# Optimization experiments

Hardware: AMD Instinct MI355X
Metric: run time of the kernel (lower is better)

## Reference

```python
import jax, jax.numpy as jnp
import numpy as np

MAX_DISP = 24  # 192 // (2**(3+1)/2**1)


def build_cost_volume(feat_l, feat_r, max_disp=MAX_DISP):
    # Faithful to the torch loop: cost[:, d, :, x] = sum_c |feat_l[..,x] - feat_r[..,x-d]|
    # with feat_r treated as zero for x < d (matches feat_l.abs().sum(1) branch).
    B, C, h, w = feat_l.shape
    pad = jnp.pad(feat_r, ((0, 0), (0, 0), (0, 0), (max_disp - 1, 0)))  # zero left-pad
    # idx[d, x] = x - d shifted into padded coords; x-d < 0 hits the zero pad.
    idx = (max_disp - 1) + jnp.arange(w)[None, :] - jnp.arange(max_disp)[:, None]  # [D, w]
    shifted = pad[:, :, :, idx]  # [B, C, h, D, w]
    cost = jnp.abs(feat_l[:, :, :, None, :] - shifted).sum(axis=1)  # [B, h, D, w]
    return jnp.transpose(cost, (0, 2, 1, 3))  # [B, D, h, w]


def bilinear_resize_align_corners(x, H, W):
    # F.interpolate(mode='bilinear', align_corners=True)
    B, C, h, w = x.shape
    ys = jnp.linspace(0.0, h - 1.0, H)
    xs = jnp.linspace(0.0, w - 1.0, W)
    y0 = jnp.floor(ys).astype(jnp.int32)
    y1 = jnp.minimum(y0 + 1, h - 1)
    wy = (ys - y0)[:, None]                 # [H, 1]
    x0 = jnp.floor(xs).astype(jnp.int32)
    x1 = jnp.minimum(x0 + 1, w - 1)
    wx = xs - x0                             # [W]
    rows = x[:, :, y0, :] * (1.0 - wy) + x[:, :, y1, :] * wy   # [B, C, H, w]
    out = rows[:, :, :, x0] * (1.0 - wx) + rows[:, :, :, x1] * wx  # [B, C, H, W]
    return out


def setup_inputs() -> dict:
    key = jax.random.key(0)
    k1, k2 = jax.random.split(key)
    B, C, h, w = 16, 4, 128, 240  # features at 1/8 of a 1024x1920 stereo pair
    feat_l = jax.random.normal(k1, (B, C, h, w), dtype=jnp.float32)
    feat_r = jax.random.normal(k2, (B, C, h, w), dtype=jnp.float32)
    return {"feat_l": feat_l, "feat_r": feat_r, "img_h": 1024, "img_w": 1920}


def reference(feat_l, feat_r, img_h, img_w):
    cost = build_cost_volume(feat_l, feat_r)            # [B, D, h, w]
    p = jax.nn.softmax(-cost, axis=1)                   # softmax over disparity bins
    disp = jnp.arange(MAX_DISP, dtype=feat_l.dtype).reshape(1, -1, 1, 1)
    pred = jnp.sum(p * disp, axis=1, keepdims=True)     # [B, 1, h, w]
    pred = pred * (float(img_h) / pred.shape[2])        # rescale disparity to full-res units
    return bilinear_resize_align_corners(pred, img_h, img_w)  # [B, 1, img_h, img_w]
```

## Files before the change

kernel.cpp:

```cpp
#include <hip/hip_runtime.h>
#include <math.h>

#define BB 16
#define CC 4
#define HH 128
#define WW 240
#define MAXD 24
#define OH 1024
#define OW 1920

__global__ __launch_bounds__(256) void fused_kernel(const float* __restrict__ fl,
                                                    const float* __restrict__ fr,
                                                    float* __restrict__ out) {
    const int blk = blockIdx.x;
    const int b = blk >> 7;
    const int y0 = blk & (HH - 1);
    const int y1 = min(y0 + 1, HH - 1);
    const int tid = threadIdx.x;

    __shared__ union {
        float sR[2][CC][WW + MAXD - 1];
        float vx[2][OW];
    } u;
    __shared__ float sP[2][WW];

    const int rows2[2] = {y0, y1};

    float lv[2][CC];
    #pragma unroll
    for (int t = 0; t < 2; ++t) {
        const int j = tid + t * 256;
        if (j < 2 * WW) {
            const int r = j / WW;
            const int x = j - r * WW;
            const size_t g = (((size_t)b * CC) * HH + rows2[r]) * WW + x;
            #pragma unroll
            for (int c = 0; c < CC; ++c)
                lv[t][c] = fl[g + (size_t)c * HH * WW];
        }
    }

    for (int i = tid; i < 2 * CC * WW; i += 256) {
        const int r = i / (CC * WW);
        const int rem = i - r * (CC * WW);
        const int c = rem / WW;
        const int x = rem - c * WW;
        u.sR[r][c][x + MAXD - 1] = fr[(((size_t)b * CC + c) * HH + rows2[r]) * WW + x];
    }
    for (int i = tid; i < 2 * CC * (MAXD - 1); i += 256) {
        const int r = i / (CC * (MAXD - 1));
        const int rem = i - r * (CC * (MAXD - 1));
        const int c = rem / (MAXD - 1);
        const int x = rem - c * (MAXD - 1);
        u.sR[r][c][x] = 0.0f;
    }
    __syncthreads();

    #pragma unroll
    for (int t = 0; t < 2; ++t) {
        const int j = tid + t * 256;
        if (j >= 2 * WW) break;
        const int r = j / WW;
        const int x = j - r * WW;
        float cost[MAXD];
        float m = 1e30f;
#pragma unroll
        for (int d = 0; d < MAXD; ++d) {
            const int xi = x - d + MAXD - 1;
            const float cv = fabsf(lv[t][0] - u.sR[r][0][xi])
                           + fabsf(lv[t][1] - u.sR[r][1][xi])
                           + fabsf(lv[t][2] - u.sR[r][2][xi])
                           + fabsf(lv[t][3] - u.sR[r][3][xi]);
            cost[d] = cv;
            m = fminf(m, cv);
        }
        float s = 0.0f, wsum = 0.0f;
#pragma unroll
        for (int d = 0; d < MAXD; ++d) {
            const float p = __expf(m - cost[d]);
            s += p;
            wsum += p * (float)d;
        }
        sP[r][x] = 8.0f * (wsum / s);
    }
    __syncthreads();

    const float sxf = (float)(WW - 1) / (float)(OW - 1);
    for (int i = tid; i < 2 * OW; i += 256) {
        const int r = i / OW;
        const int ox = i - r * OW;
        const float xsf = (float)ox * sxf;
        int x0 = (int)xsf;
        if (x0 > WW - 1) x0 = WW - 1;
        const int x1 = min(x0 + 1, WW - 1);
        const float wx = xsf - (float)x0;
        const float a = sP[r][x0];
        u.vx[r][ox] = a + (sP[r][x1] - a) * wx;
    }
    __syncthreads();

    const float syf = (float)(HH - 1) / (float)(OH - 1);
    const int base = (int)((float)y0 * ((float)(OH - 1) / (float)(HH - 1))) - 2;
    const float4* __restrict__ v0p = (const float4*)u.vx[0];
    const float4* __restrict__ v1p = (const float4*)u.vx[1];
    for (int k = 0; k < 13; ++k) {
        const int oy = base + k;
        if (oy < 0 || oy >= OH) continue;
        const float ysf = (float)oy * syf;
        int yy = (int)ysf;
        if (yy > HH - 1) yy = HH - 1;
        if (yy != y0) continue;
        const float wy = ysf - (float)yy;
        float4* __restrict__ orow = (float4*)(out + ((size_t)b * OH + oy) * OW);
        for (int q = tid; q < OW / 4; q += 256) {
            const float4 v0 = v0p[q];
            const float4 v1 = v1p[q];
            float4 o;
            o.x = v0.x + (v1.x - v0.x) * wy;
            o.y = v0.y + (v1.y - v0.y) * wy;
            o.z = v0.z + (v1.z - v0.z) * wy;
            o.w = v0.w + (v1.w - v0.w) * wy;
            orow[q] = o;
        }
    }
}

extern "C" void kernel_launch(void* const* d_in, const int* in_sizes, int n_in,
                              void* d_out, int out_size, void* d_ws, size_t ws_size,
                              hipStream_t stream) {
    const float* feat_l = (const float*)d_in[0];
    const float* feat_r = (const float*)d_in[1];
    float* out = (float*)d_out;
    fused_kernel<<<BB * HH, 256, 0, stream>>>(feat_l, feat_r, out);
}
```

Baseline: 150.2 us.

## Use 512 threads, keep interpolated row in registers, float4 smem, drop softmax max

Blocks now run 512 threads, so each thread handles one cost pixel. The right-feature rows are stored as float4 per x, so each disparity needs only one LDS.128. The softmax skips the max-subtraction pass and accumulates exp(-cost) in a single loop. Each thread keeps its horizontally interpolated output values in registers, which removes the vx shared buffer and one barrier. Dropping the max shift risks underflow if costs are large, though with costs of a few units this is unlikely.

```diff
diff --git a/kernel.cpp b/kernel.cpp
--- a/kernel.cpp
+++ b/kernel.cpp
@@ -9,100 +9,83 @@
 #define OH 1024
 #define OW 1920
 
-__global__ __launch_bounds__(256) void fused_kernel(const float* __restrict__ fl,
-                                                    const float* __restrict__ fr,
-                                                    float* __restrict__ out) {
+__global__ __launch_bounds__(512, 8) void fused_kernel(const float* __restrict__ fl,
+                                                       const float* __restrict__ fr,
+                                                       float* __restrict__ out) {
     const int blk = blockIdx.x;
     const int b = blk >> 7;
     const int y0 = blk & (HH - 1);
     const int y1 = min(y0 + 1, HH - 1);
     const int tid = threadIdx.x;
 
-    __shared__ union {
-        float sR[2][CC][WW + MAXD - 1];
-        float vx[2][OW];
-    } u;
+    __shared__ float4 sR[2][WW + MAXD - 1];
     __shared__ float sP[2][WW];
 
-    const int rows2[2] = {y0, y1};
+    const bool act = tid < 2 * WW;
+    const int pr = (tid < WW) ? 0 : 1;
+    const int px = (tid < WW) ? tid : tid - WW;
+    const int prow = pr ? y1 : y0;
 
-    float lv[2][CC];
-    #pragma unroll
-    for (int t = 0; t < 2; ++t) {
-        const int j = tid + t * 256;
-        if (j < 2 * WW) {
-            const int r = j / WW;
-            const int x = j - r * WW;
-            const size_t g = (((size_t)b * CC) * HH + rows2[r]) * WW + x;
-            #pragma unroll
-            for (int c = 0; c < CC; ++c)
-                lv[t][c] = fl[g + (size_t)c * HH * WW];
-        }
+    float4 l4 = make_float4(0.f, 0.f, 0.f, 0.f);
+    if (act) {
+        const size_t g = (((size_t)b * CC) * HH + prow) * WW + px;
+        l4.x = fl[g];
+        l4.y = fl[g + (size_t)HH * WW];
+        l4.z = fl[g + (size_t)2 * HH * WW];
+        l4.w = fl[g + (size_t)3 * HH * WW];
     }
 
-    for (int i = tid; i < 2 * CC * WW; i += 256) {
-        const int r = i / (CC * WW);
-        const int rem = i - r * (CC * WW);
-        const int c = rem / WW;
-        const int x = rem - c * WW;
-        u.sR[r][c][x + MAXD - 1] = fr[(((size_t)b * CC + c) * HH + rows2[r]) * WW + x];
+    for (int i = tid; i < 2 * CC * WW; i += 512) {
+        const int r = (i < CC * WW) ? 0 : 1;
+        const int rem = (i < CC * WW) ? i : i - CC * WW;
+        const int x = rem >> 2;
+        const int c = rem & 3;
+        const int row = r ? y1 : y0;
+        ((float*)&sR[r][MAXD - 1 + x])[c] =
+            fr[(((size_t)b * CC + c) * HH + row) * WW + x];
     }
-    for (int i = tid; i < 2 * CC * (MAXD - 1); i += 256) {
-        const int r = i / (CC * (MAXD - 1));
-        const int rem = i - r * (CC * (MAXD - 1));
-        const int c = rem / (MAXD - 1);
-        const int x = rem - c * (MAXD - 1);
-        u.sR[r][c][x] = 0.0f;
+    if (tid < 2 * CC * (MAXD - 1)) {
+        const int r = (tid < CC * (MAXD - 1)) ? 0 : 1;
+        const int rem = (tid < CC * (MAXD - 1)) ? tid : tid - CC * (MAXD - 1);
+        ((float*)&sR[r][0])[rem] = 0.0f;
     }
     __syncthreads();
 
-    #pragma unroll
-    for (int t = 0; t < 2; ++t) {
-        const int j = tid + t * 256;
-        if (j >= 2 * WW) break;
-        const int r = j / WW;
-        const int x = j - r * WW;
-        float cost[MAXD];
-        float m = 1e30f;
+    if (act) {
+        float s = 0.0f, ws = 0.0f;
 #pragma unroll
         for (int d = 0; d < MAXD; ++d) {
-            const int xi = x - d + MAXD - 1;
-            const float cv = fabsf(lv[t][0] - u.sR[r][0][xi])
-                           + fabsf(lv[t][1] - u.sR[r][1][xi])
-                           + fabsf(lv[t][2] - u.sR[r][2][xi])
-                           + fabsf(lv[t][3] - u.sR[r][3][xi]);
-            cost[d] = cv;
-            m = fminf(m, cv);
+            const float4 r4 = sR[pr][MAXD - 1 + px - d];
+            const float cv = fabsf(l4.x - r4.x) + fabsf(l4.y - r4.y)
+                           + fabsf(l4.z - r4.z) + fabsf(l4.w - r4.w);
+            const float p = __expf(-cv);
+            s += p;
+            ws += p * (float)d;
         }
-        float s = 0.0f, wsum = 0.0f;
-#pragma unroll
-        for (int d = 0; d < MAXD; ++d) {
-            const float p = __expf(m - cost[d]);
-            s += p;
-            wsum += p * (float)d;
-        }
-        sP[r][x] = 8.0f * (wsum / s);
+        sP[pr][px] = 8.0f * (ws / s);
     }
     __syncthreads();
 
     const float sxf = (float)(WW - 1) / (float)(OW - 1);
-    for (int i = tid; i < 2 * OW; i += 256) {
-        const int r = i / OW;
-        const int ox = i - r * OW;
-        const float xsf = (float)ox * sxf;
-        int x0 = (int)xsf;
-        if (x0 > WW - 1) x0 = WW - 1;
-        const int x1 = min(x0 + 1, WW - 1);
-        const float wx = xsf - (float)x0;
-        const float a = sP[r][x0];
-        u.vx[r][ox] = a + (sP[r][x1] - a) * wx;
+    float ax[4], bx[4];
+    if (act) {
+#pragma unroll
+        for (int j = 0; j < 4; ++j) {
+            const int ox = tid * 4 + j;
+            const float xsf = (float)ox * sxf;
+            int x0 = (int)xsf;
+            if (x0 > WW - 1) x0 = WW - 1;
+            const int x1 = min(x0 + 1, WW - 1);
+            const float wx = xsf - (float)x0;
+            const float p0 = sP[0][x0], q0 = sP[0][x1];
+            const float p1 = sP[1][x0], q1 = sP[1][x1];
+            ax[j] = p0 + (q0 - p0) * wx;
+            bx[j] = p1 + (q1 - p1) * wx;
+        }
     }
-    __syncthreads();
 
     const float syf = (float)(HH - 1) / (float)(OH - 1);
     const int base = (int)((float)y0 * ((float)(OH - 1) / (float)(HH - 1))) - 2;
-    const float4* __restrict__ v0p = (const float4*)u.vx[0];
-    const float4* __restrict__ v1p = (const float4*)u.vx[1];
     for (int k = 0; k < 13; ++k) {
         const int oy = base + k;
         if (oy < 0 || oy >= OH) continue;
@@ -111,16 +94,13 @@
         if (yy > HH - 1) yy = HH - 1;
         if (yy != y0) continue;
         const float wy = ysf - (float)yy;
-        float4* __restrict__ orow = (float4*)(out + ((size_t)b * OH + oy) * OW);
-        for (int q = tid; q < OW / 4; q += 256) {
-            const float4 v0 = v0p[q];
-            const float4 v1 = v1p[q];
+        if (act) {
             float4 o;
-            o.x = v0.x + (v1.x - v0.x) * wy;
-            o.y = v0.y + (v1.y - v0.y) * wy;
-            o.z = v0.z + (v1.z - v0.z) * wy;
-            o.w = v0.w + (v1.w - v0.w) * wy;
-            orow[q] = o;
+            o.x = ax[0] + (bx[0] - ax[0]) * wy;
+            o.y = ax[1] + (bx[1] - ax[1]) * wy;
+            o.z = ax[2] + (bx[2] - ax[2]) * wy;
+            o.w = ax[3] + (bx[3] - ax[3]) * wy;
+            ((float4*)(out + ((size_t)b * OH + oy) * OW))[tid] = o;
         }
     }
 }
@@ -131,5 +111,5 @@
     const float* feat_l = (const float*)d_in[0];
     const float* feat_r = (const float*)d_in[1];
     float* out = (float*)d_out;
-    fused_kernel<<<BB * HH, 256, 0, stream>>>(feat_l, feat_r, out);
+    fused_kernel<<<BB * HH, 512, 0, stream>>>(feat_l, feat_r, out);
 }
```

After: 148.1 us. About the same (-1.4%).
